# Kernel optimization log

Measured on AMD Instinct MI355X. Metric: run time of the kernel, lower is better.

Reference implementation:

```python
import jax, jax.numpy as jnp
import numpy as np

C = 1.0
MIN = 1e-15
PROJ_EPS = 4e-3  # fp32 ball-projection eps (HGCN convention)

def _artanh(x):
    x = jnp.clip(x, -1.0 + 1e-7, 1.0 - 1e-7)
    return 0.5 * jnp.log((1.0 + x) / (1.0 - x))

def _nrm(x):
    return jnp.clip(jnp.sqrt(jnp.sum(x * x, -1, keepdims=True)), MIN)

def proj(x, c=C):
    n = _nrm(x)
    maxn = (1.0 - PROJ_EPS) / jnp.sqrt(c)
    return jnp.where(n > maxn, x / n * maxn, x)

def expmap0(u, c=C):
    sc = jnp.sqrt(c); n = _nrm(u)
    return jnp.tanh(sc * n) * u / (sc * n)

def logmap0(p, c=C):
    sc = jnp.sqrt(c); n = _nrm(p)
    return _artanh(sc * n) * p / (sc * n)

def mobius_add(x, y, c=C):
    x2 = jnp.sum(x * x, -1, keepdims=True)
    y2 = jnp.sum(y * y, -1, keepdims=True)
    xy = jnp.sum(x * y, -1, keepdims=True)
    num = (1.0 + 2.0 * c * xy + c * y2) * x + (1.0 - c * x2) * y
    den = 1.0 + 2.0 * c * xy + c * c * x2 * y2
    return num / jnp.clip(den, MIN)

def logmap(p1, p2, c=C):
    # log at base p1 of p2
    sub = mobius_add(-p1, p2, c)
    sn = _nrm(sub); sc = jnp.sqrt(c)
    lam = jnp.clip(2.0 / (1.0 - c * jnp.sum(p1 * p1, -1, keepdims=True)), MIN)
    return (2.0 / (sc * lam)) * _artanh(sc * sn) * sub / sn

def expmap(u, p, c=C):
    # exp of tangent u at base p
    sc = jnp.sqrt(c); un = _nrm(u)
    lam = jnp.clip(2.0 / (1.0 - c * jnp.sum(p * p, -1, keepdims=True)), MIN)
    second = jnp.tanh(sc * lam * un / 2.0) * u / (sc * un)
    return mobius_add(p, second, c)

def mobius_matvec(M, x, c=C):
    sc = jnp.sqrt(c)
    xn = _nrm(x)
    mx = x @ M.T
    mxn = _nrm(mx)
    res = jnp.tanh(mxn / xn * _artanh(sc * xn)) * mx / (mxn * sc)
    zero = jnp.all(mx == 0.0, -1, keepdims=True)
    return jnp.where(zero, jnp.zeros_like(res), res)

def hyp_linear(x, W, b, c=C):
    res = proj(mobius_matvec(W, x, c), c)
    hb = proj(expmap0(b, c), c)
    return proj(mobius_add(res, hb, c), c)

def setup_inputs() -> dict:
    key = jax.random.key(0)
    ks = jax.random.split(key, 8)
    B, n, s, d = 2048, 1, 16, 64
    pt = lambda k, shp: proj(0.05 * jax.random.normal(k, shp, dtype=jnp.float32))
    return {
        "self_vectors": pt(ks[0], (B, n, d)),
        "ngh_user_vectors": pt(ks[1], (B, s, d)),
        "ngh_entity_vectors": pt(ks[2], (B, n, s, d)),
        "item_embeddings": pt(ks[3], (B, d)),
        "Wr": 0.05 * jax.random.normal(ks[4], (B, n, s, d, d), dtype=jnp.float32),
        "W_ui": 0.05 * jax.random.normal(ks[5], (d, d), dtype=jnp.float32),
        "lin_W": 0.05 * jax.random.normal(ks[6], (d, d), dtype=jnp.float32),
        "lin_b": 0.05 * jax.random.normal(ks[7], (d,), dtype=jnp.float32),
    }

def reference(self_vectors, ngh_user_vectors, ngh_entity_vectors, item_embeddings, Wr, W_ui, lin_W, lin_b):
    B, n, d = self_vectors.shape  # n == 1 for item layer
    s = ngh_user_vectors.shape[1]
    # ---- entity-side attention + aggregation ----
    t_self = logmap0(self_vectors)                      # [B,n,d]
    t_engh = logmap0(ngh_entity_vectors)                # [B,n,s,d]
    sWr = jnp.einsum('bnc,bnsrc->bnsr', t_self, Wr)     # sum(self*Wr, -1)
    att = jax.nn.softmax(jnp.einsum('bnsr,bnsr->bns', sWr, t_engh), axis=-1)[..., None]
    ngh_log = logmap(self_vectors[:, :, None, :], ngh_entity_vectors)  # [B,n,s,d]
    kg_agg = expmap(jnp.sum(att * ngh_log, axis=2), self_vectors)      # [B,n,d]
    # ---- user-side attention + aggregation ----
    iv = item_embeddings[:, None, :]                    # [B,1,d]
    t_item = logmap0(iv)
    t_ungh = logmap0(ngh_user_vectors)
    imW = jnp.einsum('bod,rd->bor', t_item, W_ui)       # [B,1,d]
    u_att = jax.nn.softmax(jnp.sum(imW * t_ungh, -1), axis=-1)[..., None]  # [B,s,1]
    u_log = logmap(iv, ngh_user_vectors)                # [B,s,d]
    user_agg = expmap(jnp.sum(u_att * u_log, axis=1, keepdims=True), iv)   # [B,1,d]
    # ---- 'sum' aggregation + hyperbolic linear + activation ----
    out = mobius_add(mobius_add(self_vectors, kg_agg), user_agg)
    out = hyp_linear(out.reshape(-1, d), lin_W, lin_b).reshape(B, n, d)
    out = expmap0(jnp.tanh(logmap0(out)))
    return out
```

## Files before the change

### kernel.cpp

```cpp
#include <hip/hip_runtime.h>

#define MINV 1e-15f
#define MAXNRM 0.996f

__device__ __forceinline__ float wsum(float v) {
#pragma unroll
    for (int m = 32; m; m >>= 1) v += __shfl_xor(v, m, 64);
    return v;
}

__device__ __forceinline__ float artanhf_(float x) {
    x = fminf(fmaxf(x, -1.0f + 1e-7f), 1.0f - 1e-7f);
    return 0.5f * logf((1.0f + x) / (1.0f - x));
}

#define MATVEC4(q, d0, v, acc)                                              \
    acc += (q).x * __shfl((v), (d0) + 0, 64)                                \
         + (q).y * __shfl((v), (d0) + 1, 64)                                \
         + (q).z * __shfl((v), (d0) + 2, 64)                                \
         + (q).w * __shfl((v), (d0) + 3, 64);

__global__ __launch_bounds__(256) void logits_kernel(
    const float* __restrict__ self_v,
    const float* __restrict__ ent_v,
    const float* __restrict__ Wr,
    float* __restrict__ scratch)
{
    __shared__ float sE[1024];
    __shared__ float st[64];
    const int b = blockIdx.x, tid = threadIdx.x, lane = tid & 63, wv = tid >> 6;

    for (int i = tid; i < 1024; i += 256)
        sE[i] = ent_v[(size_t)b * 1024 + i];
    if (wv == 0) {
        float xl = self_v[(size_t)b * 64 + lane];
        float x2 = wsum(xl * xl);
        float xn = fmaxf(sqrtf(x2), MINV);
        st[lane] = artanhf_(xn) / xn * xl;
    }
    __syncthreads();

    const float4* wp = (const float4*)(Wr + (size_t)b * 65536);
    const int r0 = lane >> 4;
    const int c0 = (lane & 15) * 4;
    const float t0 = st[c0], t1 = st[c0 + 1], t2 = st[c0 + 2], t3 = st[c0 + 3];

    for (int s = wv; s < 16; s += 4) {
        const float4* sp = wp + s * 1024;
        float ax = 0.f, ay = 0.f, az = 0.f, aw = 0.f;
#pragma unroll
        for (int j = 0; j < 16; ++j) {
            float4 q = sp[j * 64 + lane];
            float er = sE[s * 64 + j * 4 + r0];
            ax += q.x * er; ay += q.y * er; az += q.z * er; aw += q.w * er;
        }
        float dp = wsum(ax * t0 + ay * t1 + az * t2 + aw * t3);
        if (lane == 0) scratch[(size_t)b * 64 + s] = dp;
    }
}

__global__ __launch_bounds__(256) void tail_kernel(
    const float* __restrict__ self_v,
    const float* __restrict__ user_v,
    const float* __restrict__ ent_v,
    const float* __restrict__ item_e,
    const float* __restrict__ Wui,
    const float* __restrict__ linW,
    const float* __restrict__ linb,
    float* __restrict__ out)
{
    __shared__ float sE[1024], sU[1024];
    __shared__ float sSub[16][64];
    __shared__ float sUSub[16][64];
    __shared__ float sLog[16], sULog[16];
    __shared__ float sImw[64];
    __shared__ float sHb[64];
    __shared__ float sH2;

    const int b = blockIdx.x, tid = threadIdx.x, lane = tid & 63, wv = tid >> 6;

    for (int i = tid; i < 1024; i += 256) {
        sE[i] = ent_v[(size_t)b * 1024 + i];
        sU[i] = user_v[(size_t)b * 1024 + i];
    }

    const float xl = self_v[(size_t)b * 64 + lane];
    const float x2 = wsum(xl * xl);
    const float ivl = item_e[(size_t)b * 64 + lane];
    const float i2 = wsum(ivl * ivl);

    if (wv == 3) {
        float inn = fmaxf(sqrtf(i2), MINV);
        float til = artanhf_(inn) / inn * ivl;
        float imw = 0.f;
        const float4* wq = (const float4*)Wui;
#pragma unroll
        for (int j = 0; j < 16; ++j) {
            float4 q = wq[lane * 16 + j];
            MATVEC4(q, j * 4, til, imw)
        }
        sImw[lane] = imw;
    } else if (wv == 2) {
        float bl = linb[lane];
        float bn = fmaxf(sqrtf(wsum(bl * bl)), MINV);
        float hb = tanhf(bn) * bl / bn;
        float hn = fmaxf(sqrtf(wsum(hb * hb)), MINV);
        if (hn > MAXNRM) hb = hb / hn * MAXNRM;
        sHb[lane] = hb;
        float h2 = wsum(hb * hb);
        if (lane == 0) sH2 = h2;
    }
    __syncthreads();

    {
        const float imw = sImw[lane];
        const float omx2 = 1.f - x2;
        const float omi2 = 1.f - i2;
#pragma unroll
        for (int q = 0; q < 4; ++q) {
            const int s = wv * 4 + q;
            float el = sE[s * 64 + lane];
            float ul = sU[s * 64 + lane];
            float e2  = wsum(el * el);
            float dxe = wsum(xl * el);
            float u2  = wsum(ul * ul);
            float dxy = wsum(ivl * ul);
            float ur  = wsum(imw * ul);

            float en = fmaxf(sqrtf(e2), MINV);
            if (lane == 0)
                sLog[s] = artanhf_(en) / en * out[(size_t)b * 64 + s];
            float den  = fmaxf(1.f - 2.f * dxe + x2 * e2, MINV);
            float subl = ((1.f - 2.f * dxe + e2) * (-xl) + omx2 * el) / den;

            float unr = fmaxf(sqrtf(u2), MINV);
            if (lane == 0)
                sULog[s] = artanhf_(unr) / unr * ur;
            float uden = fmaxf(1.f - 2.f * dxy + i2 * u2, MINV);
            float usub = ((1.f - 2.f * dxy + u2) * (-ivl) + omi2 * ul) / uden;

            float sn  = fmaxf(sqrtf(wsum(subl * subl)), MINV);
            float usn = fmaxf(sqrtf(wsum(usub * usub)), MINV);
            sSub[s][lane]  = artanhf_(sn) / sn * subl;
            sUSub[s][lane] = artanhf_(usn) / usn * usub;
        }
    }
    __syncthreads();
    if (wv != 0) return;

    float mx = -1e30f, umx = -1e30f;
#pragma unroll
    for (int s = 0; s < 16; ++s) {
        mx = fmaxf(mx, sLog[s]);
        umx = fmaxf(umx, sULog[s]);
    }
    float se = 0.f, usum = 0.f, aggl = 0.f, uaggl = 0.f;
#pragma unroll
    for (int s = 0; s < 16; ++s) {
        float e = expf(sLog[s] - mx);
        se += e; aggl += e * sSub[s][lane];
        float ue = expf(sULog[s] - umx);
        usum += ue; uaggl += ue * sUSub[s][lane];
    }
    float lam  = fmaxf(2.f / (1.f - x2), MINV);
    float lami = fmaxf(2.f / (1.f - i2), MINV);
    aggl  *= (2.f / lam) / se;
    uaggl *= (2.f / lami) / usum;

    float un  = fmaxf(sqrtf(wsum(aggl * aggl)), MINV);
    float uun = fmaxf(sqrtf(wsum(uaggl * uaggl)), MINV);
    float secl = tanhf(lam * un * 0.5f) * aggl / un;
    float usec = tanhf(lami * uun * 0.5f) * uaggl / uun;

    float ss2 = wsum(secl * secl), xss = wsum(xl * secl);
    float us2 = wsum(usec * usec), uxs = wsum(ivl * usec);
    float kgl = ((1.f + 2.f * xss + ss2) * xl + (1.f - x2) * secl)
              / fmaxf(1.f + 2.f * xss + x2 * ss2, MINV);
    float ual = ((1.f + 2.f * uxs + us2) * ivl + (1.f - i2) * usec)
              / fmaxf(1.f + 2.f * uxs + i2 * us2, MINV);

    float k2 = wsum(kgl * kgl), xk = wsum(xl * kgl);
    float o1 = ((1.f + 2.f * xk + k2) * xl + (1.f - x2) * kgl)
             / fmaxf(1.f + 2.f * xk + x2 * k2, MINV);
    float o12 = wsum(o1 * o1), ua2 = wsum(ual * ual), o1u = wsum(o1 * ual);
    float v   = ((1.f + 2.f * o1u + ua2) * o1 + (1.f - o12) * ual)
              / fmaxf(1.f + 2.f * o1u + o12 * ua2, MINV);

    float v2 = wsum(v * v);
    float vn = fmaxf(sqrtf(v2), MINV);
    float mxv = 0.f;
    {
        const float4* wq = (const float4*)linW;
#pragma unroll
        for (int j = 0; j < 16; ++j) {
            float4 q = wq[lane * 16 + j];
            MATVEC4(q, j * 4, v, mxv)
        }
    }
    float mxn = fmaxf(sqrtf(wsum(mxv * mxv)), MINV);
    float res = tanhf(mxn / vn * artanhf_(vn)) * mxv / mxn;
    if (__ballot(mxv != 0.f) == 0ull) res = 0.f;
    float rn = fmaxf(sqrtf(wsum(res * res)), MINV);
    if (rn > MAXNRM) res = res / rn * MAXNRM;

    float hb = sHb[lane];
    float h2 = sH2;
    float r2 = wsum(res * res), rh = wsum(res * hb);
    float o3 = ((1.f + 2.f * rh + h2) * res + (1.f - r2) * hb)
             / fmaxf(1.f + 2.f * rh + r2 * h2, MINV);
    float on = fmaxf(sqrtf(wsum(o3 * o3)), MINV);
    if (on > MAXNRM) o3 = o3 / on * MAXNRM;

    float on2 = fmaxf(sqrtf(wsum(o3 * o3)), MINV);
    float tl  = tanhf(artanhf_(on2) / on2 * o3);
    float tn  = fmaxf(sqrtf(wsum(tl * tl)), MINV);
    out[(size_t)b * 64 + lane] = tanhf(tn) * tl / tn;
}

extern "C" void kernel_launch(void* const* d_in, const int* in_sizes, int n_in,
                              void* d_out, int out_size, void* d_ws, size_t ws_size,
                              hipStream_t stream) {
    const float* self_v = (const float*)d_in[0];
    const float* user_v = (const float*)d_in[1];
    const float* ent_v  = (const float*)d_in[2];
    const float* item_e = (const float*)d_in[3];
    const float* Wr     = (const float*)d_in[4];
    const float* Wui    = (const float*)d_in[5];
    const float* linW   = (const float*)d_in[6];
    const float* linb   = (const float*)d_in[7];
    float* out = (float*)d_out;

    const int B = in_sizes[0] / 64;

    logits_kernel<<<B, 256, 0, stream>>>(self_v, ent_v, Wr, out);
    tail_kernel<<<B, 256, 0, stream>>>(self_v, user_v, ent_v, item_e,
                                       Wui, linW, linb, out);
}
```

Before: 725.9 us.

## Split logits kernel into one block per (batch, neighbor) pair with upfront Wr loads

```diff
diff --git a/kernel.cpp b/kernel.cpp
--- a/kernel.cpp
+++ b/kernel.cpp
@@ -26,37 +26,44 @@
     const float* __restrict__ Wr,
     float* __restrict__ scratch)
 {
-    __shared__ float sE[1024];
-    __shared__ float st[64];
-    const int b = blockIdx.x, tid = threadIdx.x, lane = tid & 63, wv = tid >> 6;
-
-    for (int i = tid; i < 1024; i += 256)
-        sE[i] = ent_v[(size_t)b * 1024 + i];
+    __shared__ float sEr[64];
+    __shared__ float sT[64];
+    __shared__ float sRed[4];
+    __shared__ float sScale;
+
+    const int blk = blockIdx.x, b = blk >> 4, s = blk & 15;
+    const int t = threadIdx.x, lane = t & 63, wv = t >> 6;
+
+    const float4* wp = (const float4*)(Wr + (size_t)b * 65536 + (size_t)s * 4096);
+    float4 q0 = wp[t];
+    float4 q1 = wp[t + 256];
+    float4 q2 = wp[t + 512];
+    float4 q3 = wp[t + 768];
+
     if (wv == 0) {
+        float el = ent_v[(size_t)b * 1024 + s * 64 + lane];
+        sEr[lane] = el;
+        float en = fmaxf(sqrtf(wsum(el * el)), MINV);
+        if (lane == 0) sScale = artanhf_(en) / en;
+    } else if (wv == 1) {
         float xl = self_v[(size_t)b * 64 + lane];
-        float x2 = wsum(xl * xl);
-        float xn = fmaxf(sqrtf(x2), MINV);
-        st[lane] = artanhf_(xn) / xn * xl;
-    }
-    __syncthreads();
-
-    const float4* wp = (const float4*)(Wr + (size_t)b * 65536);
-    const int r0 = lane >> 4;
-    const int c0 = (lane & 15) * 4;
-    const float t0 = st[c0], t1 = st[c0 + 1], t2 = st[c0 + 2], t3 = st[c0 + 3];
-
-    for (int s = wv; s < 16; s += 4) {
-        const float4* sp = wp + s * 1024;
-        float ax = 0.f, ay = 0.f, az = 0.f, aw = 0.f;
-#pragma unroll
-        for (int j = 0; j < 16; ++j) {
-            float4 q = sp[j * 64 + lane];
-            float er = sE[s * 64 + j * 4 + r0];
-            ax += q.x * er; ay += q.y * er; az += q.z * er; aw += q.w * er;
-        }
-        float dp = wsum(ax * t0 + ay * t1 + az * t2 + aw * t3);
-        if (lane == 0) scratch[(size_t)b * 64 + s] = dp;
-    }
+        float xn = fmaxf(sqrtf(wsum(xl * xl)), MINV);
+        sT[lane] = artanhf_(xn) / xn * xl;
+    }
+    __syncthreads();
+
+    const float4 ts = ((const float4*)sT)[t & 15];
+    const int r0 = t >> 4;
+    float p = sEr[r0]      * (q0.x * ts.x + q0.y * ts.y + q0.z * ts.z + q0.w * ts.w)
+            + sEr[r0 + 16] * (q1.x * ts.x + q1.y * ts.y + q1.z * ts.z + q1.w * ts.w)
+            + sEr[r0 + 32] * (q2.x * ts.x + q2.y * ts.y + q2.z * ts.z + q2.w * ts.w)
+            + sEr[r0 + 48] * (q3.x * ts.x + q3.y * ts.y + q3.z * ts.z + q3.w * ts.w);
+    p = wsum(p);
+    if (lane == 0) sRed[wv] = p;
+    __syncthreads();
+    if (t == 0)
+        scratch[(size_t)b * 64 + s] =
+            sScale * (sRed[0] + sRed[1] + sRed[2] + sRed[3]);
 }
 
 __global__ __launch_bounds__(256) void tail_kernel(
@@ -83,6 +90,7 @@
         sE[i] = ent_v[(size_t)b * 1024 + i];
         sU[i] = user_v[(size_t)b * 1024 + i];
     }
+    if (tid < 16) sLog[tid] = out[(size_t)b * 64 + tid];
 
     const float xl = self_v[(size_t)b * 64 + lane];
     const float x2 = wsum(xl * xl);
@@ -121,15 +129,12 @@
             const int s = wv * 4 + q;
             float el = sE[s * 64 + lane];
             float ul = sU[s * 64 + lane];
-            float e2  = wsum(el * el);
             float dxe = wsum(xl * el);
             float u2  = wsum(ul * ul);
             float dxy = wsum(ivl * ul);
             float ur  = wsum(imw * ul);
-
-            float en = fmaxf(sqrtf(e2), MINV);
-            if (lane == 0)
-                sLog[s] = artanhf_(en) / en * out[(size_t)b * 64 + s];
+            float e2  = wsum(el * el);
+
             float den  = fmaxf(1.f - 2.f * dxe + x2 * e2, MINV);
             float subl = ((1.f - 2.f * dxe + e2) * (-xl) + omx2 * el) / den;
 
@@ -232,7 +237,7 @@
 
     const int B = in_sizes[0] / 64;
 
-    logits_kernel<<<B, 256, 0, stream>>>(self_v, ent_v, Wr, out);
+    logits_kernel<<<B * 16, 256, 0, stream>>>(self_v, ent_v, Wr, out);
     tail_kernel<<<B, 256, 0, stream>>>(self_v, user_v, ent_v, item_e,
                                        Wui, linW, linb, out);
 }
```

New measurement: 724.1 us. Within noise of the previous version (-0.2%).
